# Performance work log

Hardware: AMD Instinct MI355X
Metric: run time of the kernel (lower is better)

## Reference

```python
import jax, jax.numpy as jnp
import numpy as np

B = 256          # batch
H = 1024         # conditioning_size (dec_hid_dim)
D = 256          # gst_dim
G = 32           # num_gst
C = 16           # num_cells
O = 256          # output_size


def setup_inputs() -> dict:
    key = jax.random.key(0)
    ks = jax.random.split(key, 7)
    hidden = jax.random.normal(ks[0], (B, H), dtype=jnp.float32)
    # per-cell embedding tables: nn.Embedding(num_gst, gst_dim) stacked over cells
    gst_emb = jax.random.normal(ks[1], (C, G, D), dtype=jnp.float32)
    # per-cell Linear(gst_dim + cond, cond): weight [H, H + D] (torch [out, in]), bias [H]
    attn_w = jax.random.normal(ks[2], (C, H, H + D), dtype=jnp.float32) * 0.02
    attn_b = jax.random.normal(ks[3], (C, H), dtype=jnp.float32) * 0.02
    # per-cell v: Parameter(torch.rand(cond))
    v = jax.random.uniform(ks[4], (C, H), dtype=jnp.float32)
    # out Linear(gst_dim, output_size)
    out_w = jax.random.normal(ks[5], (O, D), dtype=jnp.float32) * 0.02
    out_b = jax.random.normal(ks[6], (O,), dtype=jnp.float32) * 0.02
    return {"hidden": hidden, "gst_emb": gst_emb, "attn_w": attn_w,
            "attn_b": attn_b, "v": v, "out_w": out_w, "out_b": out_b}


def reference(hidden, gst_emb, attn_w, attn_b, v, out_w, out_b):
    # Original concatenates (hidden, encoder_outputs) along features; split the
    # linear weight accordingly instead of materializing the concat.
    w_hid = attn_w[:, :, :H]        # [C, H, H]
    w_enc = attn_w[:, :, H:]        # [C, H, D]
    # embedding lookup of arange(G) == the table rows themselves (same for all batch)
    enc = gst_emb                   # [C, G, D]
    hid_part = jnp.einsum('bh,coh->bco', hidden, w_hid)     # [B, C, Ho]
    enc_part = jnp.einsum('cgd,cod->cgo', enc, w_enc)       # [C, G, Ho]
    energy = jnp.tanh(hid_part[:, :, None, :] + enc_part[None]
                      + attn_b[None, :, None, :])           # [B, C, G, Ho]
    scores = jnp.einsum('bcgh,ch->bcg', energy, v)          # [B, C, G]
    attention = jax.nn.softmax(scores, axis=-1)             # softmax over num_gst
    weighted = jnp.einsum('bcg,cgd->bcd', attention, enc)   # [B, C, D]
    att_cat = attention.reshape(B, C * G)                   # torch.cat(att_list, dim=1)
    pooled = jnp.mean(weighted, axis=1)                     # [B, D]
    out = pooled @ out_w.T + out_b                          # [B, O]
    return (att_cat, out)
```

## Files before the change

### kernel.cpp

```cpp
#include <hip/hip_runtime.h>
#include <hip/hip_bf16.h>

#define B_  256
#define H_  1024
#define D_  256
#define G_  32
#define C_  16
#define O_  256
#define HD_ 1280
#define N1_ 16384

typedef __attribute__((ext_vector_type(8)))  short short8;
typedef __attribute__((ext_vector_type(4)))  short s16x4;
typedef __attribute__((ext_vector_type(4)))  float f32x4;
typedef __attribute__((ext_vector_type(16))) float f32x16;

#define MFMA32(a, b, c) __builtin_amdgcn_mfma_f32_32x32x16_bf16((a), (b), (c), 0, 0, 0)

__device__ __forceinline__ float tanh_c(float x) {
    float y = __expf(2.f * x);
    float t = 1.f - 2.f * __builtin_amdgcn_rcpf(y + 1.f);
    return fminf(fmaxf(t, -0.99999994f), 0.99999994f);
}

__device__ __forceinline__ short bfhi(float x) {
    return (short)(__float_as_uint(x) >> 16);
}
__device__ __forceinline__ short bflo(float x) {
    float fhi = __uint_as_float(__float_as_uint(x) & 0xFFFF0000u);
    return (short)(__float_as_uint(x - fhi) >> 16);
}

__device__ __forceinline__ void split4(const float4 v, s16x4& hi, s16x4& lo) {
    hi[0] = bfhi(v.x); lo[0] = bflo(v.x);
    hi[1] = bfhi(v.y); lo[1] = bflo(v.y);
    hi[2] = bfhi(v.z); lo[2] = bflo(v.z);
    hi[3] = bfhi(v.w); lo[3] = bflo(v.w);
}

__global__ __launch_bounds__(256, 2) void gemm1_kernel(
    const short* __restrict__ hidH, const short* __restrict__ hidL,
    const float* __restrict__ attn_w, const float* __restrict__ attn_b,
    float* __restrict__ hp)
{
    const int tid  = threadIdx.x;
    const int wave = tid >> 6, lane = tid & 63;
    const int l31 = lane & 31;
    const int kh  = (lane >> 5) * 8;

    const int n0 = blockIdx.y * 64 + (wave & 1) * 32;
    const int s0 = blockIdx.x * 4 + (wave >> 1) * 2;

    f32x16 acc0, acc1;
    #pragma unroll
    for (int i = 0; i < 16; ++i) { acc0[i] = 0.f; acc1[i] = 0.f; }

    const size_t aBase = (size_t)s0 * 32768 + (size_t)lane * 8;
    const short* pH0 = hidH + aBase;
    const short* pH1 = hidH + aBase + 32768;
    const short* pL0 = hidL + aBase;
    const short* pL1 = hidL + aBase + 32768;

    const float* pBr = attn_w + (size_t)(n0 + l31) * HD_ + kh;

    short8 aH0[3][2], aH1[3][2], aL0[3][2], aL1[3][2];
    float4 rb[3][4];

#define LOADA(SET, KS)                                                        \
    {                                                                         \
        const int o_ = (KS) * 1024;                                           \
        aH0[SET][0] = *(const short8*)(pH0 + o_);                             \
        aH0[SET][1] = *(const short8*)(pH0 + o_ + 512);                       \
        aH1[SET][0] = *(const short8*)(pH1 + o_);                             \
        aH1[SET][1] = *(const short8*)(pH1 + o_ + 512);                       \
        aL0[SET][0] = *(const short8*)(pL0 + o_);                             \
        aL0[SET][1] = *(const short8*)(pL0 + o_ + 512);                       \
        aL1[SET][0] = *(const short8*)(pL1 + o_);                             \
        aL1[SET][1] = *(const short8*)(pL1 + o_ + 512);                       \
    }
#define LOADB(SET, KS)                                                        \
    {                                                                         \
        const float* p_ = pBr + (KS) * 32;                                    \
        rb[SET][0] = *(const float4*)(p_);                                    \
        rb[SET][1] = *(const float4*)(p_ + 4);                                \
        rb[SET][2] = *(const float4*)(p_ + 16);                               \
        rb[SET][3] = *(const float4*)(p_ + 20);                               \
    }

    LOADB(0, 0) LOADA(0, 0)
    LOADB(1, 1) LOADA(1, 1)
    LOADB(2, 2) LOADA(2, 2)

#define BODY(P, K, DOL)                                                       \
    {                                                                         \
        short8 bh0, bl0, bh1, bl1;                                            \
        {                                                                     \
            s16x4 h0, l0, h1, l1;                                             \
            split4(rb[P][0], h0, l0); split4(rb[P][1], h1, l1);               \
            bh0 = short8{h0[0],h0[1],h0[2],h0[3],h1[0],h1[1],h1[2],h1[3]};    \
            bl0 = short8{l0[0],l0[1],l0[2],l0[3],l1[0],l1[1],l1[2],l1[3]};    \
            split4(rb[P][2], h0, l0); split4(rb[P][3], h1, l1);               \
            bh1 = short8{h0[0],h0[1],h0[2],h0[3],h1[0],h1[1],h1[2],h1[3]};    \
            bl1 = short8{l0[0],l0[1],l0[2],l0[3],l1[0],l1[1],l1[2],l1[3]};    \
        }                                                                     \
        if (DOL) LOADB(P, (K) + 3)                                            \
        __builtin_amdgcn_s_setprio(1);                                        \
        acc0 = MFMA32(aH0[P][0], bh0, acc0);                                  \
        acc1 = MFMA32(aH1[P][0], bh0, acc1);                                  \
        acc0 = MFMA32(aL0[P][0], bh0, acc0);                                  \
        acc1 = MFMA32(aL1[P][0], bh0, acc1);                                  \
        acc0 = MFMA32(aH0[P][0], bl0, acc0);                                  \
        acc1 = MFMA32(aH1[P][0], bl0, acc1);                                  \
        acc0 = MFMA32(aH0[P][1], bh1, acc0);                                  \
        acc1 = MFMA32(aH1[P][1], bh1, acc1);                                  \
        acc0 = MFMA32(aL0[P][1], bh1, acc0);                                  \
        acc1 = MFMA32(aL1[P][1], bh1, acc1);                                  \
        acc0 = MFMA32(aH0[P][1], bl1, acc0);                                  \
        acc1 = MFMA32(aH1[P][1], bl1, acc1);                                  \
        __builtin_amdgcn_s_setprio(0);                                        \
        if (DOL) LOADA(P, (K) + 3)                                            \
    }

    for (int k = 0; k < 27; k += 3) {
        BODY(0, k, 1)
        BODY(1, k + 1, 1)
        BODY(2, k + 2, 1)
    }
    BODY(0, 27, 1)
    BODY(1, 28, 1)
    BODY(2, 29, 0)
    BODY(0, 30, 0)
    BODY(1, 31, 0)
#undef BODY
#undef LOADA
#undef LOADB

    const int col  = n0 + l31;
    const float bias = attn_b[col];
    const int rbase = s0 * 32 + (lane >> 5) * 4;
    float* dcol = hp + col;
    #pragma unroll
    for (int r = 0; r < 16; ++r) {
        const int row = rbase + (r & 3) + 8 * (r >> 2);
        dcol[(size_t)row * N1_]        = tanh_c(acc0[r] + bias);
        dcol[(size_t)(row + 32) * N1_] = tanh_c(acc1[r] + bias);
    }
}

__global__ __launch_bounds__(256) void gemm2_kernel(
    const float* __restrict__ enc, const float* __restrict__ attn_w,
    const float* __restrict__ hidden, float* __restrict__ ep,
    short* __restrict__ hidH, short* __restrict__ hidL)
{
    const int tid  = threadIdx.x;
    const int wave = tid >> 6, lane = tid & 63;

    {
        const int bid = blockIdx.y * 16 + blockIdx.x;
        const int gid = bid * 256 + tid;
        if (gid < 32768) {
            const int s   = gid >> 12;
            const int k0  = (gid >> 7) & 31;
            const int ks  = (gid >> 6) & 1;
            const int ln  = gid & 63;
            const int row = s * 32 + (ln & 31);
            const int colk = k0 * 32 + ks * 16 + (ln >> 5) * 8;
            const float* src = hidden + (size_t)row * H_ + colk;
            s16x4 h0, l0, h1, l1;
            split4(*(const float4*)src, h0, l0);
            split4(*(const float4*)(src + 4), h1, l1);
            *(short8*)(hidH + (size_t)gid * 8) =
                short8{h0[0],h0[1],h0[2],h0[3],h1[0],h1[1],h1[2],h1[3]};
            *(short8*)(hidL + (size_t)gid * 8) =
                short8{l0[0],l0[1],l0[2],l0[3],l1[0],l1[1],l1[2],l1[3]};
        }
    }

    const int c  = blockIdx.y;
    const int n0 = blockIdx.x * 64 + wave * 16;
    const int l16 = lane & 15;
    const int lk  = (lane >> 4) * 8;

#define MFMA16(a, b, c) __builtin_amdgcn_mfma_f32_16x16x32_bf16((a), (b), (c), 0, 0, 0)
    f32x4 acc[2];
    acc[0] = f32x4{0.f, 0.f, 0.f, 0.f};
    acc[1] = f32x4{0.f, 0.f, 0.f, 0.f};

    const float* encp = enc + c * (G_ * D_);
    const float* wp   = attn_w + (size_t)c * H_ * HD_ + H_;

    #pragma unroll
    for (int kk = 0; kk < 8; ++kk) {
        const int k0 = kk * 32 + lk;
        short8 ah[2], al[2], bh, bl;
        #pragma unroll
        for (int mi = 0; mi < 2; ++mi) {
            const float* p = encp + (mi * 16 + l16) * D_ + k0;
            s16x4 h0, l0, h1, l1;
            split4(*(const float4*)p, h0, l0);
            split4(*(const float4*)(p + 4), h1, l1);
            ah[mi] = short8{h0[0],h0[1],h0[2],h0[3],h1[0],h1[1],h1[2],h1[3]};
            al[mi] = short8{l0[0],l0[1],l0[2],l0[3],l1[0],l1[1],l1[2],l1[3]};
        }
        {
            const float* p = wp + (size_t)(n0 + l16) * HD_ + k0;
            s16x4 h0, l0, h1, l1;
            split4(*(const float4*)p, h0, l0);
            split4(*(const float4*)(p + 4), h1, l1);
            bh = short8{h0[0],h0[1],h0[2],h0[3],h1[0],h1[1],h1[2],h1[3]};
            bl = short8{l0[0],l0[1],l0[2],l0[3],l1[0],l1[1],l1[2],l1[3]};
        }
        #pragma unroll
        for (int mi = 0; mi < 2; ++mi) {
            acc[mi] = MFMA16(ah[mi], bh, acc[mi]);
            acc[mi] = MFMA16(al[mi], bh, acc[mi]);
            acc[mi] = MFMA16(ah[mi], bl, acc[mi]);
        }
    }

    const int lr = (lane >> 4) * 4;
    #pragma unroll
    for (int mi = 0; mi < 2; ++mi) {
        const int g = mi * 16 + lr;
        const int o = n0 + l16;
        float* dst = ep + (c * G_ + g) * H_ + o;
        f32x4 vacc = acc[mi];
        dst[0]      = tanh_c(vacc[0]);
        dst[H_]     = tanh_c(vacc[1]);
        dst[2 * H_] = tanh_c(vacc[2]);
        dst[3 * H_] = tanh_c(vacc[3]);
    }
#undef MFMA16
}

__global__ __launch_bounds__(256) void attn_kernel(
    const float* __restrict__ hp, const float* __restrict__ ep,
    const float* __restrict__ v, const float* __restrict__ enc,
    float* __restrict__ out, float* __restrict__ wt)
{
    const int c  = blockIdx.x;
    const int b0 = blockIdx.y * 4;
    const int tid  = threadIdx.x;
    const int wave = tid >> 6, lane = tid & 63;

    __shared__ float s_att[4][G_];
    __shared__ float s_sc[4][G_];

    f32x4 vv[4], tav[4][4];
    const float* vrow = v + c * H_;
    #pragma unroll
    for (int j = 0; j < 4; ++j)
        vv[j] = *(const f32x4*)(vrow + lane * 4 + j * 256);
    #pragma unroll
    for (int bi = 0; bi < 4; ++bi) {
        const float* hprow = hp + (size_t)(b0 + bi) * N1_ + c * H_;
        #pragma unroll
        for (int j = 0; j < 4; ++j)
            tav[bi][j] = *(const f32x4*)(hprow + lane * 4 + j * 256);
    }

    #pragma unroll
    for (int gg = 0; gg < 8; ++gg) {
        const int g = wave * 8 + gg;
        const float* eprow = ep + (size_t)(c * G_ + g) * H_;
        float s[4] = {0.f, 0.f, 0.f, 0.f};
        #pragma unroll
        for (int j = 0; j < 4; ++j) {
            const f32x4 tb = *(const f32x4*)(eprow + lane * 4 + j * 256);
            #pragma unroll
            for (int e = 0; e < 4; ++e) {
                const float tbx = tb[e];
                const float w   = vv[j][e];
                #pragma unroll
                for (int bi = 0; bi < 4; ++bi) {
                    const float ta  = tav[bi][j][e];
                    const float num = ta + tbx;
                    const float den = fmaf(ta, tbx, 1.f);
                    s[bi] = fmaf(num * __builtin_amdgcn_rcpf(den), w, s[bi]);
                }
            }
        }
        #pragma unroll
        for (int off = 32; off > 0; off >>= 1) {
            s[0] += __shfl_down(s[0], off, 64);
            s[1] += __shfl_down(s[1], off, 64);
            s[2] += __shfl_down(s[2], off, 64);
            s[3] += __shfl_down(s[3], off, 64);
        }
        if (lane == 0) {
            s_sc[0][g] = s[0]; s_sc[1][g] = s[1];
            s_sc[2][g] = s[2]; s_sc[3][g] = s[3];
        }
    }
    __syncthreads();

    if (tid < 128) {
        const int bi = tid >> 5, g = tid & 31;
        float sv = s_sc[bi][g];
        float m = sv;
        #pragma unroll
        for (int off = 16; off > 0; off >>= 1)
            m = fmaxf(m, __shfl_xor(m, off, 32));
        const float e = __expf(sv - m);
        float sum = e;
        #pragma unroll
        for (int off = 16; off > 0; off >>= 1)
            sum += __shfl_xor(sum, off, 32);
        const float a = e / sum;
        s_att[bi][g] = a;
        out[(size_t)(b0 + bi) * (C_ * G_) + c * G_ + g] = a;
    }
    __syncthreads();

    float w0 = 0.f, w1 = 0.f, w2 = 0.f, w3 = 0.f;
    const float* encc = enc + c * (G_ * D_) + tid;
    #pragma unroll
    for (int g = 0; g < G_; ++g) {
        const float e = encc[g * D_];
        w0 = fmaf(s_att[0][g], e, w0);
        w1 = fmaf(s_att[1][g], e, w1);
        w2 = fmaf(s_att[2][g], e, w2);
        w3 = fmaf(s_att[3][g], e, w3);
    }
    wt[(size_t)((b0 + 0) * C_ + c) * D_ + tid] = w0;
    wt[(size_t)((b0 + 1) * C_ + c) * D_ + tid] = w1;
    wt[(size_t)((b0 + 2) * C_ + c) * D_ + tid] = w2;
    wt[(size_t)((b0 + 3) * C_ + c) * D_ + tid] = w3;
}

__global__ __launch_bounds__(256) void out_kernel(
    const float* __restrict__ wt, const float* __restrict__ out_w,
    const float* __restrict__ out_b, float* __restrict__ out)
{
    const int b = blockIdx.x, tid = threadIdx.x;
    __shared__ float pooled[D_];

    float s = 0.f;
    #pragma unroll
    for (int c = 0; c < C_; ++c)
        s += wt[(size_t)(b * C_ + c) * D_ + tid];
    pooled[tid] = s * (1.f / 16.f);
    __syncthreads();

    float acc = out_b[tid];
    const float* wrow = out_w + tid * D_;
    #pragma unroll 8
    for (int dc = 0; dc < 64; ++dc) {
        float4 w4 = *(const float4*)(wrow + dc * 4);
        acc += pooled[dc * 4 + 0] * w4.x;
        acc += pooled[dc * 4 + 1] * w4.y;
        acc += pooled[dc * 4 + 2] * w4.z;
        acc += pooled[dc * 4 + 3] * w4.w;
    }
    out[(size_t)B_ * (C_ * G_) + b * O_ + tid] = acc;
}

extern "C" void kernel_launch(void* const* d_in, const int* in_sizes, int n_in,
                              void* d_out, int out_size, void* d_ws, size_t ws_size,
                              hipStream_t stream) {
    const float* hidden = (const float*)d_in[0];
    const float* enc    = (const float*)d_in[1];
    const float* attn_w = (const float*)d_in[2];
    const float* attn_b = (const float*)d_in[3];
    const float* v      = (const float*)d_in[4];
    const float* out_w  = (const float*)d_in[5];
    const float* out_b  = (const float*)d_in[6];
    float* out = (float*)d_out;

    float* hp = (float*)d_ws;
    float* ep = hp + (size_t)B_ * N1_;
    float* wt = ep + (size_t)C_ * G_ * H_;
    short* hidH = (short*)(wt + (size_t)B_ * C_ * D_);
    short* hidL = hidH + (size_t)B_ * H_;

    gemm2_kernel<<<dim3(16, C_), 256, 0, stream>>>(enc, attn_w, hidden, ep, hidH, hidL);
    gemm1_kernel<<<dim3(2, 256), 256, 0, stream>>>(hidH, hidL, attn_w, attn_b, hp);
    attn_kernel<<<dim3(C_, B_ / 4), 256, 0, stream>>>(hp, ep, v, enc, out, wt);
    out_kernel<<<B_, 256, 0, stream>>>(wt, out_w, out_b, out);
}
```

Before: 230.1 us.

## Stage gemm1 weight tiles in LDS via direct global-to-LDS loads

Gemm1 is reorganised so each block owns a 32-column strip of the weight and spans all 256 batch rows across its four waves. Weight tiles are brought into a 4-slot, XOR-swizzled shared-memory ring using global_load_lds DMA and shared by all waves, where before every wave loaded its own copy into registers. The aim is to cut redundant global weight traffic and register pressure. In exchange it adds a barrier per k-step and relies on hand-tuned vmcnt wait counts, and the grid becomes one-dimensional.

```diff
diff --git a/kernel.cpp b/kernel.cpp
--- a/kernel.cpp
+++ b/kernel.cpp
@@ -43,32 +43,34 @@
     const float* __restrict__ attn_w, const float* __restrict__ attn_b,
     float* __restrict__ hp)
 {
+    __shared__ float Bsf[4][32 * 32];
+
     const int tid  = threadIdx.x;
     const int wave = tid >> 6, lane = tid & 63;
-    const int l31 = lane & 31;
-    const int kh  = (lane >> 5) * 8;
-
-    const int n0 = blockIdx.y * 64 + (wave & 1) * 32;
-    const int s0 = blockIdx.x * 4 + (wave >> 1) * 2;
+    const int l31  = lane & 31;
+    const int hi2  = (lane >> 5) * 2;
+    const int sw   = l31 & 7;
+    const int n0   = blockIdx.x * 32;
 
     f32x16 acc0, acc1;
     #pragma unroll
     for (int i = 0; i < 16; ++i) { acc0[i] = 0.f; acc1[i] = 0.f; }
 
-    const size_t aBase = (size_t)s0 * 32768 + (size_t)lane * 8;
+    const int rS = tid >> 3;
+    const int cS = (tid & 7) ^ (rS & 7);
+    const float* pBsrc = attn_w + (size_t)(n0 + rS) * HD_ + cS * 4;
+
+    const size_t aBase = (size_t)(wave * 2) * 32768 + (size_t)lane * 8;
     const short* pH0 = hidH + aBase;
     const short* pH1 = hidH + aBase + 32768;
     const short* pL0 = hidL + aBase;
     const short* pL1 = hidL + aBase + 32768;
 
-    const float* pBr = attn_w + (size_t)(n0 + l31) * HD_ + kh;
-
-    short8 aH0[3][2], aH1[3][2], aL0[3][2], aL1[3][2];
-    float4 rb[3][4];
-
-#define LOADA(SET, KS)                                                        \
+    short8 aH0[2][2], aH1[2][2], aL0[2][2], aL1[2][2];
+
+#define LOADA(SET, K)                                                         \
     {                                                                         \
-        const int o_ = (KS) * 1024;                                           \
+        const int o_ = (K) * 1024;                                            \
         aH0[SET][0] = *(const short8*)(pH0 + o_);                             \
         aH0[SET][1] = *(const short8*)(pH0 + o_ + 512);                       \
         aH1[SET][0] = *(const short8*)(pH1 + o_);                             \
@@ -78,32 +80,38 @@
         aL1[SET][0] = *(const short8*)(pL1 + o_);                             \
         aL1[SET][1] = *(const short8*)(pL1 + o_ + 512);                       \
     }
-#define LOADB(SET, KS)                                                        \
+
+#define DMAB(BUF, K)                                                          \
+    __builtin_amdgcn_global_load_lds(                                         \
+        (const __attribute__((address_space(1))) void*)(pBsrc + (K) * 32),    \
+        (__attribute__((address_space(3))) void*)(&Bsf[BUF][wave * 256]),     \
+        16, 0, 0);
+
+#define READB(BUF, KS, BH, BL)                                                \
     {                                                                         \
-        const float* p_ = pBr + (KS) * 32;                                    \
-        rb[SET][0] = *(const float4*)(p_);                                    \
-        rb[SET][1] = *(const float4*)(p_ + 4);                                \
-        rb[SET][2] = *(const float4*)(p_ + 16);                               \
-        rb[SET][3] = *(const float4*)(p_ + 20);                               \
-    }
-
-    LOADB(0, 0) LOADA(0, 0)
-    LOADB(1, 1) LOADA(1, 1)
-    LOADB(2, 2) LOADA(2, 2)
-
-#define BODY(P, K, DOL)                                                       \
+        const float* rp_ = &Bsf[BUF][l31 * 32];                               \
+        const int kc_ = (KS) * 4 + hi2;                                       \
+        float4 ca_ = *(const float4*)(rp_ + ((kc_    ) ^ sw) * 4);            \
+        float4 cb_ = *(const float4*)(rp_ + ((kc_ + 1) ^ sw) * 4);            \
+        s16x4 h0_, lo0_, h1_, lo1_;                                           \
+        split4(ca_, h0_, lo0_);                                               \
+        split4(cb_, h1_, lo1_);                                               \
+        BH = short8{h0_[0],h0_[1],h0_[2],h0_[3],h1_[0],h1_[1],h1_[2],h1_[3]}; \
+        BL = short8{lo0_[0],lo0_[1],lo0_[2],lo0_[3],                          \
+                    lo1_[0],lo1_[1],lo1_[2],lo1_[3]};                         \
+    }
+
+#define ITER(P, K, VC, DOL, DODMA)                                            \
     {                                                                         \
+        asm volatile("s_waitcnt vmcnt(" #VC ")" ::: "memory");                \
+        __builtin_amdgcn_s_barrier();                                         \
+        if (DOL) LOADA(P ^ 1, (K) + 1)                                        \
+        __builtin_amdgcn_sched_barrier(0);                                    \
+        if (DODMA) DMAB(((K) + 3) & 3, (K) + 3)                               \
+        __builtin_amdgcn_sched_barrier(0);                                    \
         short8 bh0, bl0, bh1, bl1;                                            \
-        {                                                                     \
-            s16x4 h0, l0, h1, l1;                                             \
-            split4(rb[P][0], h0, l0); split4(rb[P][1], h1, l1);               \
-            bh0 = short8{h0[0],h0[1],h0[2],h0[3],h1[0],h1[1],h1[2],h1[3]};    \
-            bl0 = short8{l0[0],l0[1],l0[2],l0[3],l1[0],l1[1],l1[2],l1[3]};    \
-            split4(rb[P][2], h0, l0); split4(rb[P][3], h1, l1);               \
-            bh1 = short8{h0[0],h0[1],h0[2],h0[3],h1[0],h1[1],h1[2],h1[3]};    \
-            bl1 = short8{l0[0],l0[1],l0[2],l0[3],l1[0],l1[1],l1[2],l1[3]};    \
-        }                                                                     \
-        if (DOL) LOADB(P, (K) + 3)                                            \
+        READB((K) & 3, 0, bh0, bl0)                                           \
+        READB((K) & 3, 1, bh1, bl1)                                           \
         __builtin_amdgcn_s_setprio(1);                                        \
         acc0 = MFMA32(aH0[P][0], bh0, acc0);                                  \
         acc1 = MFMA32(aH1[P][0], bh0, acc1);                                  \
@@ -118,26 +126,32 @@
         acc0 = MFMA32(aH0[P][1], bl1, acc0);                                  \
         acc1 = MFMA32(aH1[P][1], bl1, acc1);                                  \
         __builtin_amdgcn_s_setprio(0);                                        \
-        if (DOL) LOADA(P, (K) + 3)                                            \
-    }
-
-    for (int k = 0; k < 27; k += 3) {
-        BODY(0, k, 1)
-        BODY(1, k + 1, 1)
-        BODY(2, k + 2, 1)
-    }
-    BODY(0, 27, 1)
-    BODY(1, 28, 1)
-    BODY(2, 29, 0)
-    BODY(0, 30, 0)
-    BODY(1, 31, 0)
-#undef BODY
+    }
+
+    DMAB(0, 0)
+    DMAB(1, 1)
+    DMAB(2, 2)
+    __builtin_amdgcn_sched_barrier(0);
+    LOADA(0, 0)
+
+    ITER(0, 0, 10, 1, 1)
+    ITER(1, 1, 18, 1, 1)
+    ITER(0, 2, 26, 1, 1)
+    for (int k = 3; k <= 27; k += 2) {
+        ITER(1, k,     18, 1, 1)
+        ITER(0, k + 1, 18, 1, 1)
+    }
+    ITER(1, 29, 18, 1, 0)
+    ITER(0, 30, 17, 1, 0)
+    ITER(1, 31, 16, 0, 0)
+#undef ITER
+#undef READB
+#undef DMAB
 #undef LOADA
-#undef LOADB
 
     const int col  = n0 + l31;
     const float bias = attn_b[col];
-    const int rbase = s0 * 32 + (lane >> 5) * 4;
+    const int rbase = wave * 64 + (lane >> 5) * 4;
     float* dcol = hp + col;
     #pragma unroll
     for (int r = 0; r < 16; ++r) {
@@ -374,7 +388,7 @@
     short* hidL = hidH + (size_t)B_ * H_;
 
     gemm2_kernel<<<dim3(16, C_), 256, 0, stream>>>(enc, attn_w, hidden, ep, hidH, hidL);
-    gemm1_kernel<<<dim3(2, 256), 256, 0, stream>>>(hidH, hidL, attn_w, attn_b, hp);
+    gemm1_kernel<<<512, 256, 0, stream>>>(hidH, hidL, attn_w, attn_b, hp);
     attn_kernel<<<dim3(C_, B_ / 4), 256, 0, stream>>>(hp, ep, v, enc, out, wt);
     out_kernel<<<B_, 256, 0, stream>>>(wt, out_w, out_b, out);
 }
```

Measured after the change: 210.6 us. 8.5% less time.
